# Performance work log

Hardware: AMD Instinct MI355X
Metric: run time of the kernel (lower is better)

The kernel has to match this reference:

```python
import jax, jax.numpy as jnp
import numpy as np

Q = 10        # icosahedral diamonds
M = 128       # 2**dggrid_level
L = Q * M * M # 163840 icosahedral points
KS = 9        # kernel_size / knn neighbors


def setup_inputs() -> dict:
    key = jax.random.key(0)
    k1, k2, k3, k4 = jax.random.split(key, 4)
    b, c, h, w = 1, 128, 256, 512
    x = jax.random.normal(k1, (b, c, h, w), dtype=jnp.float32)
    codeskmin = jax.random.randint(k2, (L, KS), 0, h * w, dtype=jnp.int32)
    att_w = jax.random.normal(k3, (KS, 2, KS), dtype=jnp.float32) * 0.1
    att_b = jnp.zeros((KS,), dtype=jnp.float32)
    depth_w = jax.random.normal(k4, (c, KS), dtype=jnp.float32) * 0.1
    depth_b = jnp.zeros((c,), dtype=jnp.float32)
    gamma = jnp.ones((c,), dtype=jnp.float32)
    beta = jnp.zeros((c,), dtype=jnp.float32)
    return {"x": x, "codeskmin": codeskmin, "att_w": att_w, "att_b": att_b,
            "depth_w": depth_w, "depth_b": depth_b, "gamma": gamma, "beta": beta}


def reference(x, codeskmin, att_w, att_b, depth_w, depth_b, gamma, beta):
    b, c, h, w = x.shape
    xf = x.reshape(b, c, h * w)
    # KNN gather: (b, c, L, KS)
    xe = xf[:, :, codeskmin]
    # --- SpatialAttentionModule_v1 ---
    avg = jnp.mean(xe, axis=1)           # (b, L, KS)
    mx = jnp.max(xe, axis=1)             # (b, L, KS)
    feat = jnp.stack([avg, mx], axis=1)  # (b, 2, L, KS)
    # Conv2d(2 -> KS, kernel (1,KS), no pad): reduces neighbor axis fully
    att = jnp.einsum('bilk,oik->bol', feat, att_w) + att_b[None, :, None]  # (b, KS, L)
    att = jax.nn.sigmoid(att)
    att = att.transpose(0, 2, 1)[:, None, :, :]  # (b, 1, L, KS)
    xe = att * xe + xe
    # --- depthwise conv over neighbor axis ---
    out = jnp.einsum('bclk,ck->bcl', xe, depth_w) + depth_b[None, :, None]  # (b, c, L)
    # rearrange 'b c (q h w) -> (b q) c h w'
    out = out.reshape(b, c, Q, M, M).transpose(0, 2, 1, 3, 4).reshape(b * Q, c, M, M)
    # BatchNorm (training-mode batch stats)
    mean = jnp.mean(out, axis=(0, 2, 3), keepdims=True)
    var = jnp.var(out, axis=(0, 2, 3), keepdims=True)
    out = (out - mean) * jax.lax.rsqrt(var + 1e-5)
    out = out * gamma[None, :, None, None] + beta[None, :, None, None]
    # Swish
    out = out * jax.nn.sigmoid(out)
    return out
```

## Files before the change

kernel.cpp:

```cpp
#include <hip/hip_runtime.h>
#include <hip/hip_bf16.h>

#define HW 131072
#define NCH 128
#define KS 9
#define L_TOTAL 163840
#define LPW 16

typedef float        f32x2 __attribute__((ext_vector_type(2)));
typedef float        f32x4 __attribute__((ext_vector_type(4)));
typedef unsigned int u32x2 __attribute__((ext_vector_type(2)));

static __device__ __forceinline__ float bflo(unsigned int p) { return __uint_as_float(p << 16); }
static __device__ __forceinline__ float bfhi(unsigned int p) { return __uint_as_float(p & 0xffff0000u); }
static __device__ __forceinline__ unsigned short f2bf(float f) {
    unsigned int x = __float_as_uint(f);
    return (unsigned short)((x + 0x7fffu + ((x >> 16) & 1u)) >> 16);
}
static __device__ __forceinline__ unsigned int pack2(float a, float b) {
    return (unsigned int)f2bf(a) | ((unsigned int)f2bf(b) << 16);
}

__global__ __launch_bounds__(256) void transpose_x_kernel(
    const f32x2* __restrict__ xf,
    unsigned int* __restrict__ xT,
    float2* __restrict__ meanmaxP)
{
    __shared__ unsigned short tile[128 * 128];
    __shared__ float ps[4][128];
    __shared__ float pm[4][128];
    const int tid = threadIdx.x;
    const int lane = tid & 63;
    const int wave = tid >> 6;
    const int p0 = blockIdx.x * 128;
    const int pa = 2 * lane, pb = 2 * lane + 1;

    float s0 = 0.f, s1 = 0.f;
    float m0 = -3.4e38f, m1 = -3.4e38f;
    #pragma unroll 8
    for (int it = 0; it < 32; ++it) {
        int c = wave + (it << 2);
        f32x2 v = __builtin_nontemporal_load(&xf[(long)c * (HW / 2) + (p0 >> 1) + lane]);
        tile[pa * 128 + ((c + 2 * pa) & 127)] = f2bf(v.x);
        tile[pb * 128 + ((c + 2 * pb) & 127)] = f2bf(v.y);
        s0 += v.x; s1 += v.y;
        m0 = fmaxf(m0, v.x); m1 = fmaxf(m1, v.y);
    }
    ps[wave][pa] = s0; ps[wave][pb] = s1;
    pm[wave][pa] = m0; pm[wave][pb] = m1;
    __syncthreads();

    #pragma unroll 8
    for (int it = 0; it < 32; ++it) {
        int p = wave + (it << 2);
        int colr = (2 * lane + 2 * p) & 127;
        unsigned int d = *reinterpret_cast<const unsigned int*>(&tile[p * 128 + colr]);
        xT[(long)(p0 + p) * 64 + lane] = d;
    }
    if (tid < 128) {
        float s = ps[0][tid] + ps[1][tid] + ps[2][tid] + ps[3][tid];
        float m = fmaxf(fmaxf(pm[0][tid], pm[1][tid]), fmaxf(pm[2][tid], pm[3][tid]));
        meanmaxP[p0 + tid] = make_float2(s * 0.0078125f, m);
    }
}

__global__ __launch_bounds__(256, 7) void encoder_main_kernel(
    const unsigned int* __restrict__ xT,
    const float2* __restrict__ meanmaxP,
    const int* __restrict__ cks,
    const float* __restrict__ att_w,
    const float* __restrict__ att_b,
    const float* __restrict__ depth_w,
    const float* __restrict__ depth_b,
    unsigned int* __restrict__ ybuf,
    float* __restrict__ gsum, float* __restrict__ gsq)
{
    __shared__ __align__(16) char smem[21952];
    float* attw = (float*)smem;
    float* attb = (float*)(smem + 648);
    int*   lcks = (int*)(smem + 688);
    float* mult = (float*)(smem + 2992);
    unsigned int* tile = (unsigned int*)(smem + 5312);
    float* red  = (float*)smem;

    const int tid = threadIdx.x;
    const int lane = tid & 63;
    const int wave = tid >> 6;
    const int c0 = lane * 2, c1 = c0 + 1;
    const int base_l = blockIdx.x * 64;

    if (tid < 162) attw[tid] = att_w[tid];
    if (tid < KS) attb[tid] = att_b[tid];
    for (int j = tid; j < 64 * KS; j += 256) lcks[j] = cks[base_l * KS + j];

    float dw0[KS], dw1[KS];
    #pragma unroll
    for (int k = 0; k < KS; ++k) {
        dw0[k] = depth_w[c0 * KS + k];
        dw1[k] = depth_w[c1 * KS + k];
    }
    const float db0 = depth_b[c0], db1 = depth_b[c1];
    __syncthreads();

    {
        const int l_local = tid >> 2;
        const int sub = tid & 3;
        if (sub < 3) {
            float mean[KS], mx[KS];
            #pragma unroll
            for (int k = 0; k < KS; ++k) {
                float2 mm = meanmaxP[lcks[l_local * KS + k]];
                mean[k] = mm.x; mx[k] = mm.y;
            }
            #pragma unroll
            for (int oo = 0; oo < 3; ++oo) {
                int o = sub * 3 + oo;
                float logit = attb[o];
                #pragma unroll
                for (int k = 0; k < KS; ++k) {
                    logit = fmaf(mean[k], attw[o * 18 + k], logit);
                    logit = fmaf(mx[k],   attw[o * 18 + 9 + k], logit);
                }
                mult[l_local * KS + o] = 1.0f + 1.0f / (1.0f + __expf(-logit));
            }
        }
    }
    __syncthreads();

    float sum0 = 0.f, sum1 = 0.f, sq0 = 0.f, sq1 = 0.f;
    const int l0 = wave * LPW;

    unsigned int pv[KS], pn[KS];
    #pragma unroll
    for (int k = 0; k < KS; ++k) {
        int idx = __builtin_amdgcn_readfirstlane(lcks[l0 * KS + k]);
        pv[k] = xT[(long)idx * 64 + lane];
    }

    #pragma unroll
    for (int li = 0; li < LPW; ++li) {
        const int l_local = l0 + li;
        if (li + 1 < LPW) {
            #pragma unroll
            for (int k = 0; k < KS; ++k) {
                int idx = __builtin_amdgcn_readfirstlane(lcks[(l_local + 1) * KS + k]);
                pn[k] = xT[(long)idx * 64 + lane];
            }
        }
        float acc0 = db0, acc1 = db1;
        #pragma unroll
        for (int k = 0; k < KS; ++k) {
            float mk = mult[l_local * KS + k];
            acc0 = fmaf(bflo(pv[k]) * mk, dw0[k], acc0);
            acc1 = fmaf(bfhi(pv[k]) * mk, dw1[k], acc1);
        }
        tile[l_local * 65 + lane] = pack2(acc0, acc1);
        sum0 += acc0; sum1 += acc1;
        sq0 = fmaf(acc0, acc0, sq0);
        sq1 = fmaf(acc1, acc1, sq1);
        #pragma unroll
        for (int k = 0; k < KS; ++k) pv[k] = pn[k];
    }

    __syncthreads();
    red[0 * 256 + tid] = sum0;
    red[1 * 256 + tid] = sum1;
    red[2 * 256 + tid] = sq0;
    red[3 * 256 + tid] = sq1;
    __syncthreads();

    const int q = base_l >> 14;
    const int rp0 = (base_l & 16383) >> 1;
    #pragma unroll
    for (int it = 0; it < 16; ++it) {
        int id = it * 256 + tid;
        int c = id >> 5;
        int rp = id & 31;
        unsigned int t0 = tile[(2 * rp) * 65 + (c >> 1)];
        unsigned int t1 = tile[(2 * rp + 1) * 65 + (c >> 1)];
        unsigned short a = (c & 1) ? (unsigned short)(t0 >> 16) : (unsigned short)(t0 & 0xffff);
        unsigned short b = (c & 1) ? (unsigned short)(t1 >> 16) : (unsigned short)(t1 & 0xffff);
        unsigned int val = (unsigned int)a | ((unsigned int)b << 16);
        __builtin_nontemporal_store(val, &ybuf[(long)(q * NCH + c) * 8192 + rp0 + rp]);
    }

    const int g = tid >> 6;
    const int i = tid & 63;
    float t = red[g * 256 + i] + red[g * 256 + 64 + i] +
              red[g * 256 + 128 + i] + red[g * 256 + 192 + i];
    float* dst = (g & 2) ? gsq : gsum;
    atomicAdd(&dst[2 * i + (g & 1)], t);
}

__global__ __launch_bounds__(256) void finalize_kernel(
    const u32x2* __restrict__ ybuf,
    const float* __restrict__ gsum, const float* __restrict__ gsq,
    const float* __restrict__ gamma, const float* __restrict__ beta,
    f32x4* __restrict__ out)
{
    const long j = (long)blockIdx.x * 256 + threadIdx.x;
    const int c = (int)(j >> 12) & 127;

    const float invN = 1.0f / (float)L_TOTAL;
    const float m = gsum[c] * invN;
    const float var = gsq[c] * invN - m * m;
    const float sc = gamma[c] * rsqrtf(var + 1e-5f);
    const float sh = beta[c] - m * sc;

    u32x2 u = __builtin_nontemporal_load(&ybuf[j]);
    float z0 = fmaf(bflo(u.x), sc, sh);
    float z1 = fmaf(bfhi(u.x), sc, sh);
    float z2 = fmaf(bflo(u.y), sc, sh);
    float z3 = fmaf(bfhi(u.y), sc, sh);
    f32x4 v;
    v.x = z0 / (1.0f + __expf(-z0));
    v.y = z1 / (1.0f + __expf(-z1));
    v.z = z2 / (1.0f + __expf(-z2));
    v.w = z3 / (1.0f + __expf(-z3));
    __builtin_nontemporal_store(v, &out[j]);
}

extern "C" void kernel_launch(void* const* d_in, const int* in_sizes, int n_in,
                              void* d_out, int out_size, void* d_ws, size_t ws_size,
                              hipStream_t stream) {
    const f32x2* x_f2  = (const f32x2*)d_in[0];
    const int* cks     = (const int*)d_in[1];
    const float* aw    = (const float*)d_in[2];
    const float* ab    = (const float*)d_in[3];
    const float* dw    = (const float*)d_in[4];
    const float* db    = (const float*)d_in[5];
    const float* gm    = (const float*)d_in[6];
    const float* bt    = (const float*)d_in[7];

    char* ws = (char*)d_ws;
    unsigned int* xT   = (unsigned int*)ws;
    float2* meanmaxP   = (float2*)(ws + 33554432);
    unsigned int* ybuf = (unsigned int*)(ws + 34603008);
    float* gsum        = (float*)(ws + 34603008 + 41943040);
    float* gsq         = gsum + NCH;

    hipMemsetAsync(gsum, 0, 2 * NCH * sizeof(float), stream);

    transpose_x_kernel<<<HW / 128, 256, 0, stream>>>(x_f2, xT, meanmaxP);
    encoder_main_kernel<<<L_TOTAL / 64, 256, 0, stream>>>(
        xT, meanmaxP, cks, aw, ab, dw, db, ybuf, gsum, gsq);
    finalize_kernel<<<20480, 256, 0, stream>>>(
        (const u32x2*)ybuf, gsum, gsq, gm, bt, (f32x4*)d_out);
}
```

Measured before the change: 324.1 us.

## Move output transpose from encoder kernel into finalize kernel via LDS tile

Result: slower. 338.3 us (+4.4%).

```diff
diff --git a/kernel.cpp b/kernel.cpp
--- a/kernel.cpp
+++ b/kernel.cpp
@@ -8,7 +8,6 @@
 #define LPW 16
 
 typedef float        f32x2 __attribute__((ext_vector_type(2)));
-typedef float        f32x4 __attribute__((ext_vector_type(4)));
 typedef unsigned int u32x2 __attribute__((ext_vector_type(2)));
 
 static __device__ __forceinline__ float bflo(unsigned int p) { return __uint_as_float(p << 16); }
@@ -64,7 +63,7 @@
     }
 }
 
-__global__ __launch_bounds__(256, 7) void encoder_main_kernel(
+__global__ __launch_bounds__(256, 8) void encoder_main_kernel(
     const unsigned int* __restrict__ xT,
     const float2* __restrict__ meanmaxP,
     const int* __restrict__ cks,
@@ -75,12 +74,11 @@
     unsigned int* __restrict__ ybuf,
     float* __restrict__ gsum, float* __restrict__ gsq)
 {
-    __shared__ __align__(16) char smem[21952];
+    __shared__ __align__(16) char smem[5312];
     float* attw = (float*)smem;
     float* attb = (float*)(smem + 648);
     int*   lcks = (int*)(smem + 688);
     float* mult = (float*)(smem + 2992);
-    unsigned int* tile = (unsigned int*)(smem + 5312);
     float* red  = (float*)smem;
 
     const int tid = threadIdx.x;
@@ -130,36 +128,41 @@
     float sum0 = 0.f, sum1 = 0.f, sq0 = 0.f, sq1 = 0.f;
     const int l0 = wave * LPW;
 
-    unsigned int pv[KS], pn[KS];
+    unsigned int g[2][KS];
     #pragma unroll
     for (int k = 0; k < KS; ++k) {
         int idx = __builtin_amdgcn_readfirstlane(lcks[l0 * KS + k]);
-        pv[k] = xT[(long)idx * 64 + lane];
+        g[0][k] = xT[(long)idx * 64 + lane];
+    }
+    #pragma unroll
+    for (int k = 0; k < KS; ++k) {
+        int idx = __builtin_amdgcn_readfirstlane(lcks[(l0 + 1) * KS + k]);
+        g[1][k] = xT[(long)idx * 64 + lane];
     }
 
     #pragma unroll
     for (int li = 0; li < LPW; ++li) {
         const int l_local = l0 + li;
-        if (li + 1 < LPW) {
-            #pragma unroll
-            for (int k = 0; k < KS; ++k) {
-                int idx = __builtin_amdgcn_readfirstlane(lcks[(l_local + 1) * KS + k]);
-                pn[k] = xT[(long)idx * 64 + lane];
-            }
-        }
         float acc0 = db0, acc1 = db1;
         #pragma unroll
         for (int k = 0; k < KS; ++k) {
+            unsigned int p = g[li & 1][k];
             float mk = mult[l_local * KS + k];
-            acc0 = fmaf(bflo(pv[k]) * mk, dw0[k], acc0);
-            acc1 = fmaf(bfhi(pv[k]) * mk, dw1[k], acc1);
+            acc0 = fmaf(bflo(p) * mk, dw0[k], acc0);
+            acc1 = fmaf(bfhi(p) * mk, dw1[k], acc1);
         }
-        tile[l_local * 65 + lane] = pack2(acc0, acc1);
+        if (li + 2 < LPW) {
+            #pragma unroll
+            for (int k = 0; k < KS; ++k) {
+                int idx = __builtin_amdgcn_readfirstlane(lcks[(l_local + 2) * KS + k]);
+                g[li & 1][k] = xT[(long)idx * 64 + lane];
+            }
+        }
+        __builtin_nontemporal_store(pack2(acc0, acc1),
+                                    &ybuf[(long)(base_l + l_local) * 64 + lane]);
         sum0 += acc0; sum1 += acc1;
         sq0 = fmaf(acc0, acc0, sq0);
         sq1 = fmaf(acc1, acc1, sq1);
-        #pragma unroll
-        for (int k = 0; k < KS; ++k) pv[k] = pn[k];
     }
 
     __syncthreads();
@@ -169,55 +172,55 @@
     red[3 * 256 + tid] = sq1;
     __syncthreads();
 
-    const int q = base_l >> 14;
-    const int rp0 = (base_l & 16383) >> 1;
-    #pragma unroll
-    for (int it = 0; it < 16; ++it) {
-        int id = it * 256 + tid;
-        int c = id >> 5;
-        int rp = id & 31;
-        unsigned int t0 = tile[(2 * rp) * 65 + (c >> 1)];
-        unsigned int t1 = tile[(2 * rp + 1) * 65 + (c >> 1)];
-        unsigned short a = (c & 1) ? (unsigned short)(t0 >> 16) : (unsigned short)(t0 & 0xffff);
-        unsigned short b = (c & 1) ? (unsigned short)(t1 >> 16) : (unsigned short)(t1 & 0xffff);
-        unsigned int val = (unsigned int)a | ((unsigned int)b << 16);
-        __builtin_nontemporal_store(val, &ybuf[(long)(q * NCH + c) * 8192 + rp0 + rp]);
-    }
-
-    const int g = tid >> 6;
+    const int grp = tid >> 6;
     const int i = tid & 63;
-    float t = red[g * 256 + i] + red[g * 256 + 64 + i] +
-              red[g * 256 + 128 + i] + red[g * 256 + 192 + i];
-    float* dst = (g & 2) ? gsq : gsum;
-    atomicAdd(&dst[2 * i + (g & 1)], t);
+    float t = red[grp * 256 + i] + red[grp * 256 + 64 + i] +
+              red[grp * 256 + 128 + i] + red[grp * 256 + 192 + i];
+    float* dst = (grp & 2) ? gsq : gsum;
+    atomicAdd(&dst[2 * i + (grp & 1)], t);
 }
 
 __global__ __launch_bounds__(256) void finalize_kernel(
-    const u32x2* __restrict__ ybuf,
+    const unsigned int* __restrict__ ybuf,
     const float* __restrict__ gsum, const float* __restrict__ gsq,
     const float* __restrict__ gamma, const float* __restrict__ beta,
-    f32x4* __restrict__ out)
+    float* __restrict__ out)
 {
-    const long j = (long)blockIdx.x * 256 + threadIdx.x;
-    const int c = (int)(j >> 12) & 127;
+    __shared__ unsigned short tile[128 * 130];
+    const int tid = threadIdx.x;
+    const int lane = tid & 63;
+    const int wave = tid >> 6;
+    const int q = blockIdx.x >> 7;
+    const int r0 = (blockIdx.x & 127) * 128;
+    const int c0 = 2 * lane, c1 = c0 + 1;
+
+    const long lbase = (long)q * 16384 + r0;
+    #pragma unroll 8
+    for (int it = 0; it < 32; ++it) {
+        int r = wave + (it << 2);
+        unsigned int u = __builtin_nontemporal_load(&ybuf[(lbase + r) * 64 + lane]);
+        tile[c0 * 130 + r] = (unsigned short)(u & 0xffffu);
+        tile[c1 * 130 + r] = (unsigned short)(u >> 16);
+    }
+    __syncthreads();
 
     const float invN = 1.0f / (float)L_TOTAL;
-    const float m = gsum[c] * invN;
-    const float var = gsq[c] * invN - m * m;
-    const float sc = gamma[c] * rsqrtf(var + 1e-5f);
-    const float sh = beta[c] - m * sc;
-
-    u32x2 u = __builtin_nontemporal_load(&ybuf[j]);
-    float z0 = fmaf(bflo(u.x), sc, sh);
-    float z1 = fmaf(bfhi(u.x), sc, sh);
-    float z2 = fmaf(bflo(u.y), sc, sh);
-    float z3 = fmaf(bfhi(u.y), sc, sh);
-    f32x4 v;
-    v.x = z0 / (1.0f + __expf(-z0));
-    v.y = z1 / (1.0f + __expf(-z1));
-    v.z = z2 / (1.0f + __expf(-z2));
-    v.w = z3 / (1.0f + __expf(-z3));
-    __builtin_nontemporal_store(v, &out[j]);
+    #pragma unroll 4
+    for (int it = 0; it < 32; ++it) {
+        int c = wave + (it << 2);
+        float m = gsum[c] * invN;
+        float var = gsq[c] * invN - m * m;
+        float sc = gamma[c] * rsqrtf(var + 1e-5f);
+        float sh = beta[c] - m * sc;
+        unsigned int d = *reinterpret_cast<const unsigned int*>(&tile[c * 130 + 2 * lane]);
+        float z0 = fmaf(bflo(d), sc, sh);
+        float z1 = fmaf(bfhi(d), sc, sh);
+        f32x2 v;
+        v.x = z0 / (1.0f + __expf(-z0));
+        v.y = z1 / (1.0f + __expf(-z1));
+        __builtin_nontemporal_store(v,
+            (f32x2*)&out[((long)(q * NCH + c) << 14) + r0 + 2 * lane]);
+    }
 }
 
 extern "C" void kernel_launch(void* const* d_in, const int* in_sizes, int n_in,
@@ -244,6 +247,6 @@
     transpose_x_kernel<<<HW / 128, 256, 0, stream>>>(x_f2, xT, meanmaxP);
     encoder_main_kernel<<<L_TOTAL / 64, 256, 0, stream>>>(
         xT, meanmaxP, cks, aw, ab, dw, db, ybuf, gsum, gsq);
-    finalize_kernel<<<20480, 256, 0, stream>>>(
-        (const u32x2*)ybuf, gsum, gsq, gm, bt, (f32x4*)d_out);
-}
+    finalize_kernel<<<1280, 256, 0, stream>>>(
+        ybuf, gsum, gsq, gm, bt, (float*)d_out);
+}
```
